# Kernel tuning notes

Hardware: AMD Instinct MI355X
Metric: run time of the kernel (lower is better)

The kernel has to match this reference:

```python
import jax, jax.numpy as jnp
import numpy as np

# db3 analysis filters (pywt convention), mode='zero', J=1
DEC_LO = np.array([0.035226291882100656, -0.08544127388224149, -0.13501102001039084,
                   0.4598775021193313, 0.8068915093133388, 0.3326705529509569], dtype=np.float32)
DEC_HI = np.array([-0.3326705529509569, 0.8068915093133388, -0.4598775021193313,
                   -0.13501102001039084, 0.08544127388224149, 0.035226291882100656], dtype=np.float32)
L = 6  # filter length
DN = ('NCHW', 'OIHW', 'NCHW')


def _outer_kernels(fa, fb, C):
    # 4 separable 2D kernels (rows x cols): ll, lh, hl, hh, depthwise shape (C,1,L,L)
    ks = [np.outer(a, b) for a in (fa, fb) for b in (fa, fb)]
    return [jnp.asarray(np.broadcast_to(k.astype(np.float32), (C, 1, L, L)).copy()) for k in ks]


def dwconv(x, w, pad=1):
    return jax.lax.conv_general_dilated(x, w, (1, 1), [(pad, pad), (pad, pad)],
                                        feature_group_count=x.shape[1], dimension_numbers=DN)


def conv1x1(x, w):
    return jax.lax.conv_general_dilated(x, w, (1, 1), 'VALID', dimension_numbers=DN)


def dwt_db3(x):
    # pytorch_wavelets zero mode, even N: pad 4 each side, stride-2 correlation with
    # reversed dec filters -> out spatial N/2 + 2
    C = x.shape[1]
    ks = _outer_kernels(DEC_LO[::-1], DEC_HI[::-1], C)
    return [jax.lax.conv_general_dilated(x, k, (2, 2), [(4, 4), (4, 4)],
                                         feature_group_count=C, dimension_numbers=DN)
            for k in ks]  # ll, lh, hl, hh


def idwt_db3(bands):
    # conv_transpose(stride 2, pad L-2) == zero-insert upsample + correlate with dec filters, pad 1
    C = bands[0].shape[1]
    ks = _outer_kernels(DEC_LO, DEC_HI, C)
    out = None
    for b, k in zip(bands, ks):
        y = jax.lax.conv_general_dilated(b, k, (1, 1), [(1, 1), (1, 1)], lhs_dilation=(2, 2),
                                         feature_group_count=C, dimension_numbers=DN)
        out = y if out is None else out + y
    return out


def ssl(x, w5, w7, w9):
    # NOTE: source applies conv5 to BOTH yl and ylh (conv1 is dead code) -- preserved faithfully
    ll, lh, hl, hh = dwt_db3(x)
    return idwt_db3([dwconv(ll, w5), dwconv(lh, w5), dwconv(hl, w7), dwconv(hh, w9)])


def ln_c(x, g, b, eps=1e-5):
    # nn.LayerNorm(channels) applied over the channel dim per spatial location
    mu = jnp.mean(x, axis=1, keepdims=True)
    var = jnp.var(x, axis=1, keepdims=True)
    return (x - mu) * jax.lax.rsqrt(var + eps) * g[None, :, None, None] + b[None, :, None, None]


def _forward(x, ln1_g, ln1_b, ln2_g, ln2_b, temperature,
             w_qkv, w_qkv_dw, w_ssl5, w_ssl7, w_ssl9, w_attn_out,
             w_ffn_in, w_ffn_dw, w_ffn_out, num_heads=4):
    b, c, h, w = x.shape
    # --- MDTA (channel attention, normalized q/k fallback path) ---
    xn = ln_c(x, ln1_g, ln1_b)
    kv = dwconv(conv1x1(xn, w_qkv), w_qkv_dw)          # depthwise on 2c channels
    k_, v_ = jnp.split(kv, 2, axis=1)
    q_ = ssl(xn, w_ssl5, w_ssl7, w_ssl9)               # wavelet query
    d = c // num_heads
    q_ = q_.reshape(b, num_heads, d, h * w)
    k_ = k_.reshape(b, num_heads, d, h * w)
    v_ = v_.reshape(b, num_heads, d, h * w)
    qn = q_ / jnp.maximum(jnp.linalg.norm(q_, axis=-1, keepdims=True), 1e-12)
    kn = k_ / jnp.maximum(jnp.linalg.norm(k_, axis=-1, keepdims=True), 1e-12)
    attn = jax.nn.softmax(jnp.einsum('bhdn,bhen->bhde', qn, kn) * temperature, axis=-1)
    out = jnp.einsum('bhde,bhen->bhdn', attn, v_).reshape(b, c, h, w)
    x = x + conv1x1(out, w_attn_out)
    # --- GDFN ---
    xn2 = ln_c(x, ln2_g, ln2_b)
    y = dwconv(conv1x1(xn2, w_ffn_in), w_ffn_dw)
    y1, y2 = jnp.split(y, 2, axis=1)
    x = x + conv1x1(jax.nn.gelu(y1, approximate=False) * y2, w_ffn_out)
    return x


def setup_inputs() -> dict:
    key = jax.random.key(0)
    B, C, H, W = 4, 192, 128, 128
    HEADS = 4
    HID = int(C * 2.66)  # 510
    ks = jax.random.split(key, 12)
    s = 0.02
    return {
        'x': jax.random.normal(ks[0], (B, C, H, W), jnp.float32),
        'ln1_g': jnp.ones((C,), jnp.float32),
        'ln1_b': jnp.zeros((C,), jnp.float32),
        'ln2_g': jnp.ones((C,), jnp.float32),
        'ln2_b': jnp.zeros((C,), jnp.float32),
        'temperature': jnp.ones((1, HEADS, 1, 1), jnp.float32),
        'w_qkv': jax.random.normal(ks[1], (2 * C, C, 1, 1), jnp.float32) * s,
        'w_qkv_dw': jax.random.normal(ks[2], (2 * C, 1, 3, 3), jnp.float32) * 0.1,
        'w_ssl5': jax.random.normal(ks[3], (C, 1, 3, 3), jnp.float32) * 0.1,
        'w_ssl7': jax.random.normal(ks[4], (C, 1, 3, 3), jnp.float32) * 0.1,
        'w_ssl9': jax.random.normal(ks[5], (C, 1, 3, 3), jnp.float32) * 0.1,
        'w_attn_out': jax.random.normal(ks[6], (C, C, 1, 1), jnp.float32) * s,
        'w_ffn_in': jax.random.normal(ks[7], (2 * HID, C, 1, 1), jnp.float32) * s,
        'w_ffn_dw': jax.random.normal(ks[8], (2 * HID, 1, 3, 3), jnp.float32) * 0.1,
        'w_ffn_out': jax.random.normal(ks[9], (C, HID, 1, 1), jnp.float32) * s,
    }


def reference(x, ln1_g, ln1_b, ln2_g, ln2_b, temperature,
              w_qkv, w_qkv_dw, w_ssl5, w_ssl7, w_ssl9, w_attn_out,
              w_ffn_in, w_ffn_dw, w_ffn_out):
    return _forward(x, ln1_g, ln1_b, ln2_g, ln2_b, temperature,
                    w_qkv, w_qkv_dw, w_ssl5, w_ssl7, w_ssl9, w_attn_out,
                    w_ffn_in, w_ffn_dw, w_ffn_out)
```

## Files before the change

kernel.cpp:

```cpp
#include <hip/hip_runtime.h>
#include <math.h>

#define HWSZ 16384
#define WID 128
#define HEI 128
#define CCH 192
#define BB 4

typedef short v8s __attribute__((ext_vector_type(8)));
typedef float f32x4 __attribute__((ext_vector_type(4)));

__device__ __constant__ float c_lo[6] = {0.035226291882100656f, -0.08544127388224149f, -0.13501102001039084f,
                                         0.4598775021193313f, 0.8068915093133388f, 0.3326705529509569f};
__device__ __constant__ float c_hi[6] = {-0.3326705529509569f, 0.8068915093133388f, -0.4598775021193313f,
                                         -0.13501102001039084f, 0.08544127388224149f, 0.035226291882100656f};

__device__ __forceinline__ float b2f(unsigned short h) { return __uint_as_float(((unsigned int)h) << 16); }
__device__ __forceinline__ unsigned short f2b(float f) {
    unsigned int u = __float_as_uint(f);
    return (unsigned short)((u + 0x7fffu + ((u >> 16) & 1u)) >> 16);
}
__device__ __forceinline__ unsigned int pk2(float a, float b) {
    return (unsigned int)f2b(a) | ((unsigned int)f2b(b) << 16);
}

__device__ __forceinline__ void gl2lds16(const void* g, void* l) {
    __builtin_amdgcn_global_load_lds((const __attribute__((address_space(1))) unsigned int*)g,
                                     (__attribute__((address_space(3))) unsigned int*)l, 16, 0, 0);
}

__global__ __launch_bounds__(256) void k_wconv(const float* __restrict__ src,
    unsigned short* __restrict__ dst, int rows, int cols, int dcols, int total)
{
    int i = blockIdx.x * 256 + threadIdx.x;
    if (i >= total) return;
    int r = i / dcols, c = i - r * dcols;
    float v = (c < cols && r < rows) ? src[r * cols + c] : 0.f;
    dst[i] = f2b(v);
}

template<int WRITE_SP>
__global__ __launch_bounds__(256) void k_ln(const float* __restrict__ x,
    const float* __restrict__ g, const float* __restrict__ bta,
    unsigned short* __restrict__ xsp, unsigned short* __restrict__ xT)
{
    int pg = blockIdx.x * 256 + threadIdx.x;
    int b = pg >> 14, p = pg & 16383;
    const float* xp = x + (size_t)b * CCH * HWSZ + p;
    float s = 0.f, s2 = 0.f;
    for (int c = 0; c < CCH; ++c) {
        float v = xp[(size_t)c * HWSZ];
        s += v; s2 += v * v;
    }
    float mu = s * (1.f / CCH);
    float var = s2 * (1.f / CCH) - mu * mu;
    float rs = rsqrtf(var + 1e-5f);
    unsigned short* tr = xT + ((size_t)b * HWSZ + p) * CCH;
    unsigned short* sp = xsp + (size_t)b * CCH * HWSZ + p;
    for (int c0 = 0; c0 < CCH; c0 += 8) {
        float vv[8];
#pragma unroll
        for (int i = 0; i < 8; ++i) {
            float v = xp[(size_t)(c0 + i) * HWSZ];
            v = (v - mu) * rs * g[c0 + i] + bta[c0 + i];
            vv[i] = v;
            if (WRITE_SP) sp[(size_t)(c0 + i) * HWSZ] = f2b(v);
        }
        uint4 u;
        u.x = pk2(vv[0], vv[1]); u.y = pk2(vv[2], vv[3]);
        u.z = pk2(vv[4], vv[5]); u.w = pk2(vv[6], vv[7]);
        *(uint4*)(tr + c0) = u;
    }
}

template<int OUT_BF16, int ADD, int K, int LDW, int BM>
__global__ __launch_bounds__(256) void k_gemmT(
    const unsigned short* __restrict__ X, const unsigned short* __restrict__ W,
    void* __restrict__ outp, const float* __restrict__ addsrc,
    int Mtot, int wstrideB)
{
    constexpr int FI = BM / 32;
    constexpr int CO = BM / 2;
    __shared__ char smem[BM * 128 + 16384];
    unsigned short* Wt = (unsigned short*)smem;
    unsigned short* Xt = Wt + BM * 64;
    float* epi = (float*)smem;

    int lane = threadIdx.x & 63, wv = threadIdx.x >> 6;
    int wr = wv >> 1, wc = wv & 1;
    int r = lane & 15, koct = lane >> 4;
    int lr = lane >> 3, lc = lane & 7;
    int b = blockIdx.z;
    int pxb = blockIdx.x * 128;
    int co0 = blockIdx.y * BM;

    const unsigned short* Wbase = W + (size_t)b * wstrideB;
    const unsigned short* Xbase = X + (size_t)b * HWSZ * K;

    f32x4 z = {0.f, 0.f, 0.f, 0.f};
    f32x4 acc[FI][4];
#pragma unroll
    for (int i = 0; i < FI; ++i)
#pragma unroll
        for (int j = 0; j < 4; ++j) acc[i][j] = z;

    for (int kt = 0; kt < K / 64; ++kt) {
        int k0 = kt * 64;
#pragma unroll
        for (int m = 0; m < FI; ++m) {
            int rowb = (wv * FI + m) * 8;
            gl2lds16(Wbase + (size_t)(co0 + rowb + lr) * LDW + k0 + lc * 8, Wt + rowb * 64);
        }
#pragma unroll
        for (int m = 0; m < 4; ++m) {
            int rowb = (wv * 4 + m) * 8;
            gl2lds16(Xbase + (size_t)(pxb + rowb + lr) * K + k0 + lc * 8, Xt + rowb * 64);
        }
        __syncthreads();
#pragma unroll
        for (int ks = 0; ks < 2; ++ks) {
            v8s bfr[4];
#pragma unroll
            for (int j = 0; j < 4; ++j)
                bfr[j] = *(const v8s*)(Xt + (wc * 64 + j * 16 + r) * 64 + ks * 32 + koct * 8);
#pragma unroll
            for (int i = 0; i < FI; ++i) {
                v8s af = *(const v8s*)(Wt + (wr * CO + i * 16 + r) * 64 + ks * 32 + koct * 8);
#pragma unroll
                for (int j = 0; j < 4; ++j)
                    acc[i][j] = __builtin_amdgcn_mfma_f32_16x16x32_bf16(af, bfr[j], acc[i][j], 0, 0, 0);
            }
        }
        __syncthreads();
    }

    int cl = lane >> 3, p4 = lc * 4;
    float* ew = epi + wv * 1152;
#pragma unroll
    for (int ig = 0; ig < FI / 2; ++ig) {
#pragma unroll
        for (int p = 0; p < 2; ++p) {
            __syncthreads();
#pragma unroll
            for (int f = 0; f < 2; ++f)
#pragma unroll
                for (int jh = 0; jh < 2; ++jh)
#pragma unroll
                    for (int jj = 0; jj < 4; ++jj)
                        ew[(f * 16 + koct * 4 + jj) * 36 + jh * 16 + r] = acc[ig * 2 + f][p * 2 + jh][jj];
            __syncthreads();
#pragma unroll
            for (int cg = 0; cg < 4; ++cg) {
                int co_l = cg * 8 + cl;
                const float* lrow = ew + co_l * 36 + p4;
                float v0 = lrow[0], v1 = lrow[1], v2 = lrow[2], v3 = lrow[3];
                int co = co0 + wr * CO + ig * 32 + co_l;
                size_t oi = ((size_t)b * Mtot + co) * HWSZ + pxb + wc * 64 + p * 32 + p4;
                if (ADD) {
                    float4 a = *(const float4*)(addsrc + oi);
                    v0 += a.x; v1 += a.y; v2 += a.z; v3 += a.w;
                }
                if (OUT_BF16) {
                    uint2 u;
                    u.x = pk2(v0, v1); u.y = pk2(v2, v3);
                    *(uint2*)((unsigned short*)outp + oi) = u;
                } else {
                    float4 f4 = {v0, v1, v2, v3};
                    *(float4*)((float*)outp + oi) = f4;
                }
            }
        }
    }
}

__device__ __forceinline__ void dw_load_tile(const unsigned short* __restrict__ ip,
    int r0, float (&tile)[18][132], int tid)
{
    for (int e = tid; e < 576; e += 256) {
        int r = e >> 5, q4 = e & 31;
        int gr = r0 - 1 + r;
        float v0 = 0.f, v1 = 0.f, v2 = 0.f, v3 = 0.f;
        if (gr >= 0 && gr < HEI) {
            uint2 u = *(const uint2*)(ip + gr * WID + q4 * 4);
            const unsigned short* pu = (const unsigned short*)&u;
            v0 = b2f(pu[0]); v1 = b2f(pu[1]); v2 = b2f(pu[2]); v3 = b2f(pu[3]);
        }
        int cb = 1 + q4 * 4;
        tile[r][cb] = v0; tile[r][cb + 1] = v1; tile[r][cb + 2] = v2; tile[r][cb + 3] = v3;
    }
    if (tid < 18) { tile[tid][0] = 0.f; tile[tid][129] = 0.f; }
}

__device__ __forceinline__ void dw_compute8(const float (&tile)[18][132],
    const float* wr, int rl, int px0, float (&o)[8])
{
    float r0[10], r1[10], r2[10];
#pragma unroll
    for (int i = 0; i < 10; ++i) {
        r0[i] = tile[rl][px0 + i];
        r1[i] = tile[rl + 1][px0 + i];
        r2[i] = tile[rl + 2][px0 + i];
    }
#pragma unroll
    for (int j = 0; j < 8; ++j) {
        o[j] = r0[j] * wr[0] + r0[j + 1] * wr[1] + r0[j + 2] * wr[2]
             + r1[j] * wr[3] + r1[j + 1] * wr[4] + r1[j + 2] * wr[5]
             + r2[j] * wr[6] + r2[j + 1] * wr[7] + r2[j + 2] * wr[8];
    }
}

template<int REDUCE>
__global__ __launch_bounds__(256) void k_dw8(const unsigned short* __restrict__ in,
    const float* __restrict__ w, unsigned short* __restrict__ out, float* __restrict__ red,
    int inCtot, int inCoff, int outCtot, int outCoff)
{
    __shared__ float tile[18][132];
    int g = blockIdx.x, c = blockIdx.y, b = blockIdx.z;
    int tid = threadIdx.x;
    const unsigned short* ip = in + (size_t)(b * inCtot + inCoff + c) * HWSZ;
    dw_load_tile(ip, g * 16, tile, tid);
    float wr[9];
#pragma unroll
    for (int j = 0; j < 9; ++j) wr[j] = w[c * 9 + j];
    __syncthreads();
    int rl = tid >> 4, px0 = (tid & 15) * 8;
    float o[8];
    dw_compute8(tile, wr, rl, px0, o);
    unsigned short* op = out + (size_t)(b * outCtot + outCoff + c) * HWSZ + (g * 16 + rl) * WID + px0;
    uint4 u;
    u.x = pk2(o[0], o[1]); u.y = pk2(o[2], o[3]); u.z = pk2(o[4], o[5]); u.w = pk2(o[6], o[7]);
    *(uint4*)op = u;
    if (REDUCE) {
        float s = 0.f;
#pragma unroll
        for (int j = 0; j < 8; ++j) s += o[j] * o[j];
        for (int off = 32; off; off >>= 1) s += __shfl_down(s, off, 64);
        __shared__ float w4[4];
        if ((tid & 63) == 0) w4[tid >> 6] = s;
        __syncthreads();
        if (tid == 0) atomicAdd(red + b * CCH + c, w4[0] + w4[1] + w4[2] + w4[3]);
    }
}

__global__ __launch_bounds__(256) void k_dw8gate(const unsigned short* __restrict__ y12,
    const float* __restrict__ w1, const float* __restrict__ w2,
    unsigned short* __restrict__ out, int validc)
{
    __shared__ float t1[18][132];
    __shared__ float t2[18][132];
    int g = blockIdx.x, c = blockIdx.y, b = blockIdx.z;
    int tid = threadIdx.x;
    const unsigned short* i1 = y12 + (size_t)(b * 512 + c) * HWSZ;
    const unsigned short* i2 = y12 + (size_t)(b * 512 + 256 + c) * HWSZ;
    dw_load_tile(i1, g * 16, t1, tid);
    dw_load_tile(i2, g * 16, t2, tid);
    bool vc = (c < validc);
    float wr1[9], wr2[9];
#pragma unroll
    for (int j = 0; j < 9; ++j) {
        wr1[j] = vc ? w1[c * 9 + j] : 0.f;
        wr2[j] = vc ? w2[c * 9 + j] : 0.f;
    }
    __syncthreads();
    int rl = tid >> 4, px0 = (tid & 15) * 8;
    float a[8], bg[8];
    dw_compute8(t1, wr1, rl, px0, a);
    dw_compute8(t2, wr2, rl, px0, bg);
    float o[8];
#pragma unroll
    for (int j = 0; j < 8; ++j)
        o[j] = 0.5f * a[j] * (1.f + erff(a[j] * 0.70710678118654752f)) * bg[j];
    unsigned short* op = out + (size_t)(b * 256 + c) * HWSZ + (g * 16 + rl) * WID + px0;
    uint4 u;
    u.x = pk2(o[0], o[1]); u.y = pk2(o[2], o[3]); u.z = pk2(o[4], o[5]); u.w = pk2(o[6], o[7]);
    *(uint4*)op = u;
}

template<int CT>
__global__ __launch_bounds__(256) void k_transT(const unsigned short* __restrict__ in,
    unsigned short* __restrict__ outT, int inCtot, int inCoff, int ldo, int coff)
{
    __shared__ unsigned short lt[64 * CT];
    const int NG = CT / 8;
    int px0 = blockIdx.x * 64, b = blockIdx.z;
    for (int idx = threadIdx.x; idx < 8 * CT; idx += 256) {
        int ch = idx >> 3, chunk = idx & 7;
        uint4 u = *(const uint4*)(in + ((size_t)(b * inCtot + inCoff + ch)) * HWSZ + px0 + chunk * 8);
        const unsigned short* pu = (const unsigned short*)&u;
        int gq = ch >> 3, j = ch & 7;
#pragma unroll
        for (int i = 0; i < 8; ++i) {
            int row = chunk * 8 + i;
            int gs = gq ^ (row >> 3);
            lt[row * CT + gs * 8 + j] = pu[i];
        }
    }
    __syncthreads();
    for (int idx = threadIdx.x; idx < 8 * CT; idx += 256) {
        int px = idx / NG, cc = idx - px * NG;
        int gs = cc ^ (px >> 3);
        uint4 v = *(const uint4*)&lt[px * CT + gs * 8];
        *(uint4*)(outT + ((size_t)b * HWSZ + px0 + px) * ldo + coff + cc * 8) = v;
    }
}

__global__ __launch_bounds__(256) void k_dwt_row(const unsigned short* __restrict__ xnb,
    unsigned short* __restrict__ rowbuf)
{
    int bc = blockIdx.x;
    const unsigned short* ip = xnb + (size_t)bc * HWSZ;
    unsigned short* lo = rowbuf + (size_t)bc * 9216;
    unsigned short* hi = rowbuf + (size_t)(768 + bc) * 9216;
    for (int idx = threadIdx.x; idx < 128 * 66; idx += 256) {
        int row = idx / 66, ow = idx - row * 66;
        const unsigned short* rp = ip + row * 128;
        int base = 2 * ow - 4;
        float v[6];
#pragma unroll
        for (int j = 0; j < 6; ++j) {
            int iw = base + j;
            v[j] = (iw >= 0 && iw < 128) ? b2f(rp[iw]) : 0.f;
        }
        float lv = 0.f, hv = 0.f;
#pragma unroll
        for (int j = 0; j < 6; ++j) {
            lv += v[j] * c_lo[5 - j];
            hv += v[j] * c_hi[5 - j];
        }
        lo[row * 72 + ow] = f2b(lv); hi[row * 72 + ow] = f2b(hv);
    }
}

__global__ __launch_bounds__(256) void k_dwt_colconv(const unsigned short* __restrict__ rowbuf,
    const float* __restrict__ w5, const float* __restrict__ w7, const float* __restrict__ w9,
    unsigned short* __restrict__ bfilt)
{
    __shared__ unsigned short rb[136][72];
    __shared__ float bnd[68][68];
    int h = blockIdx.x, c = blockIdx.y, b = blockIdx.z;
    int tid = threadIdx.x;
    int bc = b * CCH + c;
    const unsigned short* src = rowbuf + (size_t)(h * 768 + bc) * 9216;
    for (int e = tid; e < 1224; e += 256) {
        int r = e / 9, qd = e - r * 9;
        int gr = r - 4;
        uint4 u = make_uint4(0, 0, 0, 0);
        if (gr >= 0 && gr < 128) u = *(const uint4*)(src + gr * 72 + qd * 8);
        *(uint4*)&rb[r][qd * 8] = u;
    }
    for (int e = tid; e < 268; e += 256) {
        int rr, cc;
        if (e < 68) { rr = 0; cc = e; }
        else if (e < 136) { rr = 67; cc = e - 68; }
        else if (e < 202) { rr = e - 135; cc = 0; }
        else { rr = e - 201; cc = 67; }
        bnd[rr][cc] = 0.f;
    }
    __syncthreads();
    for (int fs = 0; fs < 2; ++fs) {
        int band = fs * 2 + h;
        const float* fa = fs ? c_hi : c_lo;
        float f5[6];
#pragma unroll
        for (int j = 0; j < 6; ++j) f5[j] = fa[5 - j];
        for (int i = tid; i < 4356; i += 256) {
            int oh = i / 66, ow = i - oh * 66;
            float a = 0.f;
#pragma unroll
            for (int ki = 0; ki < 6; ++ki)
                a += f5[ki] * b2f(rb[oh * 2 + ki][ow]);
            bnd[oh + 1][ow + 1] = a;
        }
        __syncthreads();
        const float* wsel = (band < 2) ? w5 : (band == 2 ? w7 : w9);
        float wr[9];
#pragma unroll
        for (int j = 0; j < 9; ++j) wr[j] = wsel[c * 9 + j];
        unsigned short* op = bfilt + ((size_t)bc * 4 + band) * 4356;
        for (int i = tid; i < 2178; i += 256) {
            int oh = i / 33, p2 = i - oh * 33;
            int ow0 = p2 * 2;
            float t[3][4];
#pragma unroll
            for (int dy = 0; dy < 3; ++dy)
#pragma unroll
                for (int dx = 0; dx < 4; ++dx)
                    t[dy][dx] = bnd[oh + dy][ow0 + dx];
            float o0 = t[0][0] * wr[0] + t[0][1] * wr[1] + t[0][2] * wr[2]
                     + t[1][0] * wr[3] + t[1][1] * wr[4] + t[1][2] * wr[5]
                     + t[2][0] * wr[6] + t[2][1] * wr[7] + t[2][2] * wr[8];
            float o1 = t[0][1] * wr[0] + t[0][2] * wr[1] + t[0][3] * wr[2]
                     + t[1][1] * wr[3] + t[1][2] * wr[4] + t[1][3] * wr[5]
                     + t[2][1] * wr[6] + t[2][2] * wr[7] + t[2][3] * wr[8];
            *(unsigned int*)(op + oh * 66 + ow0) = pk2(o0, o1);
        }
        __syncthreads();
    }
}

__global__ __launch_bounds__(256) void k_idwt2(const unsigned short* __restrict__ bfilt,
    unsigned short* __restrict__ q, float* __restrict__ rq2)
{
    __shared__ float L[4][10][68];
    __shared__ float w4[4];
    int g = blockIdx.x;
    int c = blockIdx.y, b = blockIdx.z;
    int tid = threadIdx.x;
    int bc = b * CCH + c;
    const unsigned short* bp = bfilt + (size_t)bc * 4 * 4356;
    for (int e = tid; e < 1320; e += 256) {
        int idx = e * 2;
        int band = idx / 660, rem = idx - band * 660;
        int rr = rem / 66, cc = rem - rr * 66;
        unsigned int u = *(const unsigned int*)(bp + band * 4356 + (8 * g + rr) * 66 + cc);
        L[band][rr][cc] = b2f((unsigned short)(u & 0xffffu));
        L[band][rr][cc + 1] = b2f((unsigned short)(u >> 16));
    }
    __syncthreads();
    int rl = tid >> 4, px0 = (tid & 15) * 8;
    int oh = 16 * g + rl;
    int Tl = rl >> 1, pr = rl & 1;
    int mb = px0 >> 1;
    float acc[8];
#pragma unroll
    for (int j = 0; j < 8; ++j) acc[j] = 0.f;
#pragma unroll
    for (int band = 0; band < 4; ++band) {
        const float* fv = (band < 2) ? c_lo : c_hi;
        const float* fh = (band & 1) ? c_hi : c_lo;
        float fv3[3] = {fv[1 - pr], fv[3 - pr], fv[5 - pr]};
        float fhe[3] = {fh[1], fh[3], fh[5]};
        float fho[3] = {fh[0], fh[2], fh[4]};
#pragma unroll
        for (int i = 0; i < 3; ++i) {
            float r6[6];
#pragma unroll
            for (int m = 0; m < 6; ++m) r6[m] = L[band][Tl + i][mb + m];
#pragma unroll
            for (int jj = 0; jj < 4; ++jj) {
                float se = fhe[0] * r6[jj] + fhe[1] * r6[jj + 1] + fhe[2] * r6[jj + 2];
                float so = fho[0] * r6[jj] + fho[1] * r6[jj + 1] + fho[2] * r6[jj + 2];
                acc[2 * jj]     += fv3[i] * se;
                acc[2 * jj + 1] += fv3[i] * so;
            }
        }
    }
    unsigned short* op = q + (size_t)bc * HWSZ + oh * WID + px0;
    uint4 u;
    u.x = pk2(acc[0], acc[1]); u.y = pk2(acc[2], acc[3]);
    u.z = pk2(acc[4], acc[5]); u.w = pk2(acc[6], acc[7]);
    *(uint4*)op = u;
    float s = 0.f;
#pragma unroll
    for (int j = 0; j < 8; ++j) s += acc[j] * acc[j];
    for (int off = 32; off; off >>= 1) s += __shfl_down(s, off, 64);
    if ((tid & 63) == 0) w4[tid >> 6] = s;
    __syncthreads();
    if (tid == 0) atomicAdd(rq2 + bc, w4[0] + w4[1] + w4[2] + w4[3]);
}

__global__ __launch_bounds__(256) void k_fnorm(const float* __restrict__ rq2,
    const float* __restrict__ rk2, float* __restrict__ rq, float* __restrict__ rk)
{
    int i = blockIdx.x * 256 + threadIdx.x;
    if (i < 768) rq[i] = 1.f / fmaxf(sqrtf(rq2[i]), 1e-12f);
    else if (i < 1536) rk[i - 768] = 1.f / fmaxf(sqrtf(rk2[i - 768]), 1e-12f);
}

__global__ __launch_bounds__(256) void k_qk_mfma(const unsigned short* __restrict__ q,
    const unsigned short* __restrict__ kv, float* __restrict__ pS)
{
    __shared__ float red[4][2304];
    int slice = blockIdx.x, bh = blockIdx.y;
    int b = bh >> 2, h = bh & 3;
    int wv = threadIdx.x >> 6, lane = threadIdx.x & 63;
    int r = lane & 15, koct = lane >> 4;
    const unsigned short* qb = q + (size_t)(b * CCH + h * 48) * HWSZ;
    const unsigned short* kb = kv + (size_t)(b * 384 + h * 48) * HWSZ;
    int n0 = slice * 1024 + wv * 256 + koct * 8;
    f32x4 z = {0.f, 0.f, 0.f, 0.f};
    f32x4 acc[3][3];
#pragma unroll
    for (int i = 0; i < 3; ++i)
#pragma unroll
        for (int j = 0; j < 3; ++j) acc[i][j] = z;
#pragma unroll
    for (int step = 0; step < 8; ++step) {
        int n = n0 + step * 32;
        v8s qf[3], kf[3];
#pragma unroll
        for (int i = 0; i < 3; ++i) {
            qf[i] = *(const v8s*)(qb + (size_t)(16 * i + r) * HWSZ + n);
            kf[i] = *(const v8s*)(kb + (size_t)(16 * i + r) * HWSZ + n);
        }
#pragma unroll
        for (int i = 0; i < 3; ++i)
#pragma unroll
            for (int j = 0; j < 3; ++j)
                acc[i][j] = __builtin_amdgcn_mfma_f32_16x16x32_bf16(qf[i], kf[j], acc[i][j], 0, 0, 0);
    }
#pragma unroll
    for (int i = 0; i < 3; ++i)
#pragma unroll
        for (int j = 0; j < 3; ++j)
#pragma unroll
            for (int jj = 0; jj < 4; ++jj)
                red[wv][(16 * i + koct * 4 + jj) * 48 + 16 * j + r] = acc[i][j][jj];
    __syncthreads();
    float* ps = pS + (size_t)(slice * 16 + bh) * 2304;
    for (int e = threadIdx.x; e < 2304; e += 256)
        ps[e] = red[0][e] + red[1][e] + red[2][e] + red[3][e];
}

__global__ __launch_bounds__(256) void k_attn_soft(const float* __restrict__ pS,
    const float* __restrict__ rq, const float* __restrict__ rk,
    const float* __restrict__ temp, float* __restrict__ attnw)
{
    int bh = blockIdx.x; int b = bh >> 2, h = bh & 3;
    __shared__ float S[48][49];
    int tid = threadIdx.x, dt = tid >> 4, et = tid & 15;
    float tv = temp[h];
#pragma unroll
    for (int i = 0; i < 3; ++i) {
#pragma unroll
        for (int j = 0; j < 3; ++j) {
            int d = dt + 16 * i, e = et + 16 * j;
            float s = 0.f;
            for (int sl = 0; sl < 16; ++sl)
                s += pS[(size_t)(sl * 16 + bh) * 2304 + d * 48 + e];
            S[d][e] = s * tv * rq[b * CCH + h * 48 + d] * rk[b * CCH + h * 48 + e];
        }
    }
    __syncthreads();
    if (tid < 48) {
        float mx = -1e30f;
        for (int e = 0; e < 48; ++e) mx = fmaxf(mx, S[tid][e]);
        float sum = 0.f;
        for (int e = 0; e < 48; ++e) sum += expf(S[tid][e] - mx);
        float inv = 1.f / sum;
        for (int e = 0; e < 48; ++e)
            attnw[((size_t)bh * 48 + tid) * 48 + e] = expf(S[tid][e] - mx) * inv;
    }
}

__global__ __launch_bounds__(192) void k_wfuse(const float* __restrict__ wattn,
    const float* __restrict__ attnw, unsigned short* __restrict__ wf)
{
    int co = blockIdx.x, b = blockIdx.y;
    int ce = threadIdx.x;
    int h = ce / 48, e = ce - h * 48;
    const float* wrow = wattn + (size_t)co * 192 + h * 48;
    const float* arow = attnw + ((size_t)(b * 4 + h) * 48) * 48 + e;
    float acc = 0.f;
#pragma unroll 8
    for (int d = 0; d < 48; ++d)
        acc += wrow[d] * arow[(size_t)d * 48];
    wf[((size_t)b * 192 + co) * 192 + ce] = f2b(acc);
}

extern "C" void kernel_launch(void* const* d_in, const int* in_sizes, int n_in,
                              void* d_out, int out_size, void* d_ws, size_t ws_size,
                              hipStream_t stream)
{
    const float* x     = (const float*)d_in[0];
    const float* ln1g  = (const float*)d_in[1];
    const float* ln1b  = (const float*)d_in[2];
    const float* ln2g  = (const float*)d_in[3];
    const float* ln2b  = (const float*)d_in[4];
    const float* temp  = (const float*)d_in[5];
    const float* wqkv  = (const float*)d_in[6];
    const float* wqkvd = (const float*)d_in[7];
    const float* w5    = (const float*)d_in[8];
    const float* w7    = (const float*)d_in[9];
    const float* w9    = (const float*)d_in[10];
    const float* wattn = (const float*)d_in[11];
    const float* wffni = (const float*)d_in[12];
    const float* wffnd = (const float*)d_in[13];
    const float* wffno = (const float*)d_in[14];
    float* out = (float*)d_out;

    char* ws = (char*)d_ws;
    unsigned short* xnT = (unsigned short*)(ws + 0);
    unsigned short* xnb = (unsigned short*)(ws + 25165824);
    unsigned short* q = (unsigned short*)(ws + 75497472);
    unsigned short* kvb = (unsigned short*)(ws + 100663296);
    unsigned short* bfilt = (unsigned short*)(ws + 100663296);
    unsigned short* rowbuf = (unsigned short*)(ws + 154189824);
    unsigned short* kvtmp384 = (unsigned short*)(ws + 154189824);
    const size_t SM = 226492416;
    float* rq2   = (float*)(ws + SM);
    float* rk2   = (float*)(ws + SM + 4096);
    float* rq    = (float*)(ws + SM + 8192);
    float* rk    = (float*)(ws + SM + 12288);
    float* pS    = (float*)(ws + SM + 16384);
    float* attnw = pS;
    unsigned short* wq_b  = (unsigned short*)(ws + SM + 2375680);
    unsigned short* wfi_b = (unsigned short*)(ws + SM + 2523136);
    unsigned short* wfo_b = (unsigned short*)(ws + SM + 2916352);
    unsigned short* wf_b  = (unsigned short*)(ws + SM + 3112960);
    const size_t NEED = SM + 3407872;
    if (ws_size < NEED) return;

    unsigned short* vT   = xnb;
    unsigned short* y12  = (unsigned short*)(ws + 25165824);
    unsigned short* gg   = (unsigned short*)(ws + 92274688);
    unsigned short* gTb  = (unsigned short*)(ws + 125829120);

    dim3 blk(256);

    hipMemsetAsync(ws + SM, 0, 8192, stream);
    k_wconv<<<288, blk, 0, stream>>>(wqkv, wq_b, 384, 192, 192, 73728);
    k_wconv<<<192, blk, 0, stream>>>(wffni, wfi_b, 256, 192, 192, 49152);
    k_wconv<<<192, blk, 0, stream>>>(wffni + (size_t)510 * 192, wfi_b + 256 * 192, 256, 192, 192, 49152);
    k_wconv<<<192, blk, 0, stream>>>(wffni + (size_t)256 * 192, wfi_b + 512 * 192, 254, 192, 192, 49152);
    k_wconv<<<192, blk, 0, stream>>>(wffni + (size_t)766 * 192, wfi_b + 768 * 192, 254, 192, 192, 49152);
    k_wconv<<<384, blk, 0, stream>>>(wffno, wfo_b, 192, 510, 512, 98304);

    k_ln<1><<<256, blk, 0, stream>>>(x, ln1g, ln1b, xnb, xnT);

    k_dwt_row<<<768, blk, 0, stream>>>(xnb, rowbuf);
    k_dwt_colconv<<<dim3(2, CCH, BB), blk, 0, stream>>>(rowbuf, w5, w7, w9, bfilt);
    k_idwt2<<<dim3(8, CCH, BB), blk, 0, stream>>>(bfilt, q, rq2);

    k_gemmT<1, 0, 192, 192, 128><<<dim3(128, 3, BB), blk, 0, stream>>>(xnT, wq_b, kvtmp384, nullptr, 384, 0);
    k_dw8<1><<<dim3(8, 192, BB), blk, 0, stream>>>(kvtmp384, wqkvd, kvb, rk2, 384, 0, 384, 0);
    k_dw8<0><<<dim3(8, 192, BB), blk, 0, stream>>>(kvtmp384, wqkvd + 192 * 9, kvb, nullptr, 384, 192, 384, 192);

    k_fnorm<<<6, blk, 0, stream>>>(rq2, rk2, rq, rk);
    k_qk_mfma<<<dim3(16, 16), blk, 0, stream>>>(q, kvb, pS);
    k_attn_soft<<<16, blk, 0, stream>>>(pS, rq, rk, temp, attnw);
    k_wfuse<<<dim3(192, 4), 192, 0, stream>>>(wattn, attnw, wf_b);

    k_transT<192><<<dim3(256, 1, BB), blk, 0, stream>>>(kvb, vT, 384, 192, 192, 0);
    k_gemmT<0, 1, 192, 192, 192><<<dim3(128, 1, BB), blk, 0, stream>>>(vT, wf_b, out, x, 192, 36864);

    k_ln<0><<<256, blk, 0, stream>>>(out, ln2g, ln2b, nullptr, xnT);

    for (int ck = 0; ck < 2; ++ck) {
        int validc = (ck == 0) ? 256 : 254;
        k_gemmT<1, 0, 192, 192, 128><<<dim3(128, 4, BB), blk, 0, stream>>>(xnT, wfi_b + (size_t)(ck * 512) * 192,
                                                                           y12, nullptr, 512, 0);
        k_dw8gate<<<dim3(8, 256, BB), blk, 0, stream>>>(y12, wffnd + (size_t)(ck * 256) * 9,
                                                        wffnd + (size_t)(510 + ck * 256) * 9, gg, validc);
        k_transT<256><<<dim3(256, 1, BB), blk, 0, stream>>>(gg, gTb, 256, 0, 512, ck * 256);
    }
    k_gemmT<0, 1, 512, 512, 192><<<dim3(128, 1, BB), blk, 0, stream>>>(gTb, wfo_b, out, out, 192, 0);
}
```

Measured before the change: 523.5 us.

## Split LayerNorm channel reduction across four waves with LDS partial sums

```diff
diff --git a/kernel.cpp b/kernel.cpp
--- a/kernel.cpp
+++ b/kernel.cpp
@@ -40,36 +40,49 @@
 }
 
 template<int WRITE_SP>
-__global__ __launch_bounds__(256) void k_ln(const float* __restrict__ x,
-    const float* __restrict__ g, const float* __restrict__ bta,
+__global__ __launch_bounds__(256) void k_ln2(const float* __restrict__ x,
+    const float* __restrict__ gw, const float* __restrict__ bta,
     unsigned short* __restrict__ xsp, unsigned short* __restrict__ xT)
 {
-    int pg = blockIdx.x * 256 + threadIdx.x;
-    int b = pg >> 14, p = pg & 16383;
-    const float* xp = x + (size_t)b * CCH * HWSZ + p;
+    __shared__ float ps[2][4][64];
+    int t = threadIdx.x;
+    int pxl = t & 63, g = t >> 6;
+    int blk = blockIdx.x;
+    int b = blk >> 8;
+    int px = ((blk & 255) << 6) + pxl;
+    int c0 = g * 48;
+    const float* xp = x + (size_t)b * CCH * HWSZ + px;
+    float v[48];
     float s = 0.f, s2 = 0.f;
-    for (int c = 0; c < CCH; ++c) {
-        float v = xp[(size_t)c * HWSZ];
-        s += v; s2 += v * v;
-    }
-    float mu = s * (1.f / CCH);
-    float var = s2 * (1.f / CCH) - mu * mu;
+#pragma unroll
+    for (int i = 0; i < 48; ++i) {
+        float vv = xp[(size_t)(c0 + i) * HWSZ];
+        v[i] = vv;
+        s += vv; s2 += vv * vv;
+    }
+    ps[0][g][pxl] = s; ps[1][g][pxl] = s2;
+    __syncthreads();
+    float ts = ps[0][0][pxl] + ps[0][1][pxl] + ps[0][2][pxl] + ps[0][3][pxl];
+    float ts2 = ps[1][0][pxl] + ps[1][1][pxl] + ps[1][2][pxl] + ps[1][3][pxl];
+    float mu = ts * (1.f / CCH);
+    float var = ts2 * (1.f / CCH) - mu * mu;
     float rs = rsqrtf(var + 1e-5f);
-    unsigned short* tr = xT + ((size_t)b * HWSZ + p) * CCH;
-    unsigned short* sp = xsp + (size_t)b * CCH * HWSZ + p;
-    for (int c0 = 0; c0 < CCH; c0 += 8) {
-        float vv[8];
-#pragma unroll
-        for (int i = 0; i < 8; ++i) {
-            float v = xp[(size_t)(c0 + i) * HWSZ];
-            v = (v - mu) * rs * g[c0 + i] + bta[c0 + i];
-            vv[i] = v;
-            if (WRITE_SP) sp[(size_t)(c0 + i) * HWSZ] = f2b(v);
-        }
+    unsigned short* sp = xsp + (size_t)b * CCH * HWSZ + px;
+    unsigned short* tr = xT + ((size_t)b * HWSZ + px) * CCH + c0;
+#pragma unroll
+    for (int i = 0; i < 48; ++i) {
+        float vv = (v[i] - mu) * rs * gw[c0 + i] + bta[c0 + i];
+        v[i] = vv;
+        if (WRITE_SP) sp[(size_t)(c0 + i) * HWSZ] = f2b(vv);
+    }
+#pragma unroll
+    for (int q = 0; q < 6; ++q) {
         uint4 u;
-        u.x = pk2(vv[0], vv[1]); u.y = pk2(vv[2], vv[3]);
-        u.z = pk2(vv[4], vv[5]); u.w = pk2(vv[6], vv[7]);
-        *(uint4*)(tr + c0) = u;
+        u.x = pk2(v[q * 8 + 0], v[q * 8 + 1]);
+        u.y = pk2(v[q * 8 + 2], v[q * 8 + 3]);
+        u.z = pk2(v[q * 8 + 4], v[q * 8 + 5]);
+        u.w = pk2(v[q * 8 + 6], v[q * 8 + 7]);
+        *(uint4*)(tr + q * 8) = u;
     }
 }
 
@@ -616,7 +629,7 @@
     k_wconv<<<192, blk, 0, stream>>>(wffni + (size_t)766 * 192, wfi_b + 768 * 192, 254, 192, 192, 49152);
     k_wconv<<<384, blk, 0, stream>>>(wffno, wfo_b, 192, 510, 512, 98304);
 
-    k_ln<1><<<256, blk, 0, stream>>>(x, ln1g, ln1b, xnb, xnT);
+    k_ln2<1><<<1024, blk, 0, stream>>>(x, ln1g, ln1b, xnb, xnT);
 
     k_dwt_row<<<768, blk, 0, stream>>>(xnb, rowbuf);
     k_dwt_colconv<<<dim3(2, CCH, BB), blk, 0, stream>>>(rowbuf, w5, w7, w9, bfilt);
@@ -634,7 +647,7 @@
     k_transT<192><<<dim3(256, 1, BB), blk, 0, stream>>>(kvb, vT, 384, 192, 192, 0);
     k_gemmT<0, 1, 192, 192, 192><<<dim3(128, 1, BB), blk, 0, stream>>>(vT, wf_b, out, x, 192, 36864);
 
-    k_ln<0><<<256, blk, 0, stream>>>(out, ln2g, ln2b, nullptr, xnT);
+    k_ln2<0><<<1024, blk, 0, stream>>>(out, ln2g, ln2b, nullptr, xnT);
 
     for (int ck = 0; ck < 2; ++ck) {
         int validc = (ck == 0) ? 256 : 254;
```

Measured after the change: 468.9 us. 10.4% less time.
